# Optimization experiments

Measured on AMD Instinct MI355X. Metric: run time of the kernel, lower is better.

The kernel has to match this reference:

```python
import jax, jax.numpy as jnp
import numpy as np

N = 8192      # total factor-graph rows (detection nodes + association nodes)
ND = N // 2   # detection-node rows; rest are association (edge) rows
D_RAW = 74    # raw input dim; last 10 cols = convex hull (5 points x 2 coords)
EPS = 1e-5    # BatchNorm eps


def _adjs():
    # signed factor-graph adjacencies with self-loops marking row type
    rng = np.random.RandomState(0)
    deg = 8
    node_adj = np.zeros((N, N), np.float32)
    edge_adj = np.zeros((N, N), np.float32)
    nbr = rng.randint(ND, N, size=(ND, deg))
    node_adj[np.repeat(np.arange(ND), deg), nbr.ravel()] = rng.choice([-1.0, 1.0], ND * deg).astype(np.float32)
    node_adj[np.arange(ND), np.arange(ND)] = 1.0
    nbr2 = rng.randint(0, ND, size=(N - ND, deg))
    edge_adj[np.repeat(np.arange(ND, N), deg), nbr2.ravel()] = rng.choice([-1.0, 1.0], (N - ND) * deg).astype(np.float32)
    edge_adj[np.arange(ND, N), np.arange(ND, N)] = 1.0
    return jnp.asarray(node_adj), jnp.asarray(edge_adj)


def setup_inputs() -> dict:
    key = jax.random.key(0)
    ks = jax.random.split(key, 16)
    node_adj, edge_adj = _adjs()

    def lin(k, fi, fo):
        return jax.random.normal(k, (fi, fo), jnp.float32) / np.sqrt(fi)

    inp = {"x": jax.random.normal(ks[0], (N, D_RAW), jnp.float32),
           "node_adj": node_adj, "edge_adj": edge_adj}
    # PointNetfeatsmall: 1x1 conv stack 3->16->32->64 with eval-mode BatchNorm
    for i, (fi, fo) in enumerate([(3, 16), (16, 32), (32, 64)], 1):
        k = jax.random.split(ks[i], 5)
        inp[f"pn_w{i}"] = lin(k[0], fi, fo)
        inp[f"pn_b{i}"] = 0.1 * jax.random.normal(k[1], (fo,), jnp.float32)
        inp[f"pn_g{i}"] = 1.0 + 0.1 * jax.random.normal(k[2], (fo,), jnp.float32)
        inp[f"pn_be{i}"] = 0.1 * jax.random.normal(k[3], (fo,), jnp.float32)
        inp[f"pn_m{i}"] = 0.1 * jax.random.normal(k[4], (fo,), jnp.float32)
        inp[f"pn_v{i}"] = jnp.ones((fo,), jnp.float32)
    # FactorGraphConvolution weights (msg_type='concat' -> in dim doubles)
    for i, (fi, fo) in enumerate([(256, 64), (128, 64), (128, 1)], 1):
        k = jax.random.split(ks[10 + i], 2)
        inp[f"gc{i}_wn"] = lin(k[0], fi, fo)
        inp[f"gc{i}_we"] = lin(k[1], fi, fo)
        inp[f"gc{i}_bn"] = jnp.zeros((fo,), jnp.float32)
        inp[f"gc{i}_be"] = jnp.zeros((fo,), jnp.float32)
    inp["gc3_bn"] = jnp.full((1,), -4.595, jnp.float32)  # nn.init.constant_ in TrackMPNN.__init__
    inp["gc3_be"] = jnp.full((1,), 4.595, jnp.float32)
    return inp


def _bn(h, g, b, m, v):  # h: [N, C, P], eval-mode BatchNorm1d
    return (h - m[:, None]) * (g[:, None] / jnp.sqrt(v[:, None] + EPS)) + b[:, None]


def _fgc(h, node_adj, edge_adj, wn, we, bn_, be_, relu):
    # concat(self, aggregated-neighbors) -> linear; node/edge rows use their own branch
    node_out = jnp.concatenate([h, node_adj @ h], axis=1) @ wn + bn_
    edge_out = jnp.concatenate([h, edge_adj @ h], axis=1) @ we + be_
    out = jnp.where((jnp.diag(node_adj) != 0)[:, None], node_out, edge_out)
    return jax.nn.relu(out) if relu else out


def reference(x, node_adj, edge_adj,
              pn_w1, pn_b1, pn_g1, pn_be1, pn_m1, pn_v1,
              pn_w2, pn_b2, pn_g2, pn_be2, pn_m2, pn_v2,
              pn_w3, pn_b3, pn_g3, pn_be3, pn_m3, pn_v3,
              gc1_wn, gc1_we, gc1_bn, gc1_be,
              gc2_wn, gc2_we, gc2_bn, gc2_be,
              gc3_wn, gc3_we, gc3_bn, gc3_be):
    # convex hull branch: [N, 3, 5] (third coordinate zero-padded)
    ch = jnp.concatenate([x[:, -10:].reshape(-1, 2, 5),
                          jnp.zeros((x.shape[0], 1, 5), x.dtype)], axis=1)
    h = jax.nn.relu(_bn(jnp.einsum('ncp,cd->ndp', ch, pn_w1) + pn_b1[:, None], pn_g1, pn_be1, pn_m1, pn_v1))
    h = jax.nn.relu(_bn(jnp.einsum('ncp,cd->ndp', h, pn_w2) + pn_b2[:, None], pn_g2, pn_be2, pn_m2, pn_v2))
    h = _bn(jnp.einsum('ncp,cd->ndp', h, pn_w3) + pn_b3[:, None], pn_g3, pn_be3, pn_m3, pn_v3)
    feat = h.max(axis=2)                       # PointNet global max pool -> [N, 64]
    h = jnp.concatenate([x[:, :-10], feat], axis=1)  # [N, 128]
    h = _fgc(h, node_adj, edge_adj, gc1_wn, gc1_we, gc1_bn, gc1_be, True)
    h = _fgc(h, node_adj, edge_adj, gc2_wn, gc2_we, gc2_bn, gc2_be, True)
    h = _fgc(h, node_adj, edge_adj, gc3_wn, gc3_we, gc3_bn, gc3_be, False)
    return jax.nn.sigmoid(h)                   # [N, 1]
```

## Files before the change

### kernel.cpp

```cpp
#include <hip/hip_runtime.h>
#include <math.h>

#define NROWS 8192
#define NDET  4096

static constexpr int OFF_SGN = 65536;
static constexpr int OFF_PN  = 131072;
static constexpr int OFF_AGG = 655360;
static constexpr int OFF_H1  = 1703936;
static constexpr int OFF_H2  = 2228224;

__global__ __launch_bounds__(256) void k_extract(
    const float* __restrict__ nodeA, const float* __restrict__ edgeA,
    int* __restrict__ idx, float* __restrict__ sgn)
{
    int row = blockIdx.x, t = threadIdx.x;
    const float* src; int col0;
    if (row < NDET) { src = nodeA + (size_t)row * NROWS + NDET; col0 = NDET; }
    else            { src = edgeA + (size_t)row * NROWS;        col0 = 0;    }
    __shared__ int scnt;
    if (t == 0) scnt = 0;
    __syncthreads();
    const float4* s4 = (const float4*)src;
    #pragma unroll
    for (int it = 0; it < 4; ++it) {
        float4 v = s4[t + it * 256];
        int cb = col0 + (t + it * 256) * 4;
        if (v.x != 0.f) { int p = atomicAdd(&scnt, 1); idx[row * 8 + p] = cb;     sgn[row * 8 + p] = v.x; }
        if (v.y != 0.f) { int p = atomicAdd(&scnt, 1); idx[row * 8 + p] = cb + 1; sgn[row * 8 + p] = v.y; }
        if (v.z != 0.f) { int p = atomicAdd(&scnt, 1); idx[row * 8 + p] = cb + 2; sgn[row * 8 + p] = v.z; }
        if (v.w != 0.f) { int p = atomicAdd(&scnt, 1); idx[row * 8 + p] = cb + 3; sgn[row * 8 + p] = v.w; }
    }
    __syncthreads();
    for (int p = scnt + t; p < 8; p += 256) { idx[row * 8 + p] = 0; sgn[row * 8 + p] = 0.f; }
}

__global__ __launch_bounds__(256) void k_pointnet(
    const float* __restrict__ x,
    const float* __restrict__ w1, const float* __restrict__ b1,
    const float* __restrict__ g1, const float* __restrict__ be1,
    const float* __restrict__ m1, const float* __restrict__ v1,
    const float* __restrict__ w2, const float* __restrict__ b2,
    const float* __restrict__ g2, const float* __restrict__ be2,
    const float* __restrict__ m2, const float* __restrict__ v2,
    const float* __restrict__ w3, const float* __restrict__ b3,
    const float* __restrict__ g3, const float* __restrict__ be3,
    const float* __restrict__ m3, const float* __restrict__ v3,
    float* __restrict__ pn)
{
    __shared__ float fw[2720];
    int t = threadIdx.x;
    for (int i = t; i < 48; i += 256)  { int d = i & 15; fw[i]       = w1[i] * g1[d] * rsqrtf(v1[d] + 1e-5f); }
    for (int i = t; i < 16; i += 256)  {                 fw[48 + i]  = (b1[i] - m1[i]) * g1[i] * rsqrtf(v1[i] + 1e-5f) + be1[i]; }
    for (int i = t; i < 512; i += 256) { int d = i & 31; fw[64 + i]  = w2[i] * g2[d] * rsqrtf(v2[d] + 1e-5f); }
    for (int i = t; i < 32; i += 256)  {                 fw[576 + i] = (b2[i] - m2[i]) * g2[i] * rsqrtf(v2[i] + 1e-5f) + be2[i]; }
    for (int i = t; i < 2048; i += 256){ int d = i & 63; fw[608 + i] = w3[i] * g3[d] * rsqrtf(v3[d] + 1e-5f); }
    for (int i = t; i < 64; i += 256)  {                 fw[2656 + i]= (b3[i] - m3[i]) * g3[i] * rsqrtf(v3[i] + 1e-5f) + be3[i]; }
    __syncthreads();

    int lane = t & 63;
    int wv   = t >> 6;
    int l15  = lane & 15, l31 = lane & 31;
    int rowbase = (blockIdx.x * 4 + wv) * 4;

    for (int r = rowbase; r < rowbase + 4; ++r) {
        float val  = (lane < 10) ? x[(size_t)r * 74 + 64 + lane] : 0.f;
        float vmax = -3.0e38f;
        #pragma unroll
        for (int p = 0; p < 5; ++p) {
            float a0 = __shfl(val, p, 64);
            float a1 = __shfl(val, p + 5, 64);
            float h1v = fmaxf(0.f, a0 * fw[l15] + a1 * fw[16 + l15] + fw[48 + l15]);
            float s2 = fw[576 + l31];
            #pragma unroll
            for (int d = 0; d < 16; ++d)
                s2 += __shfl(h1v, d, 64) * fw[64 + d * 32 + l31];
            float h2v = fmaxf(0.f, s2);
            float s3 = fw[2656 + lane];
            #pragma unroll
            for (int e = 0; e < 32; ++e)
                s3 += __shfl(h2v, e, 64) * fw[608 + e * 64 + lane];
            vmax = fmaxf(vmax, s3);
        }
        pn[(size_t)r * 64 + lane] = vmax;
    }
}

__global__ __launch_bounds__(256) void k_gather1(
    const float* __restrict__ x, const float* __restrict__ pn,
    const int* __restrict__ idx, const float* __restrict__ sgn,
    float* __restrict__ agg)
{
    int lane = threadIdx.x & 63;
    int row  = blockIdx.x * 4 + (threadIdx.x >> 6);
    float acc0 = x[(size_t)row * 74 + lane];
    float acc1 = pn[(size_t)row * 64 + lane];
    #pragma unroll
    for (int j = 0; j < 8; ++j) {
        int nb   = idx[row * 8 + j];
        float sg = sgn[row * 8 + j];
        acc0 += sg * x[(size_t)nb * 74 + lane];
        acc1 += sg * pn[(size_t)nb * 64 + lane];
    }
    agg[(size_t)row * 128 + lane]      = acc0;
    agg[(size_t)row * 128 + 64 + lane] = acc1;
}

__global__ __launch_bounds__(256) void k_gather2(
    const float* __restrict__ h, const int* __restrict__ idx,
    const float* __restrict__ sgn, float* __restrict__ agg)
{
    int lane = threadIdx.x & 63;
    int row  = blockIdx.x * 4 + (threadIdx.x >> 6);
    float acc = h[(size_t)row * 64 + lane];
    #pragma unroll
    for (int j = 0; j < 8; ++j) {
        int nb   = idx[row * 8 + j];
        float sg = sgn[row * 8 + j];
        acc += sg * h[(size_t)nb * 64 + lane];
    }
    agg[(size_t)row * 64 + lane] = acc;
}

__global__ __launch_bounds__(256) void k_gemm1(
    const float* __restrict__ x, const float* __restrict__ pn,
    const float* __restrict__ agg,
    const float* __restrict__ wn, const float* __restrict__ we,
    const float* __restrict__ bn, const float* __restrict__ be,
    float* __restrict__ out)
{
    int r_l = threadIdx.x >> 2, cg = threadIdx.x & 3;
    int row = blockIdx.x * 64 + r_l;
    int c0  = blockIdx.y * 16 + cg * 4;
    bool isnode = blockIdx.x < 64;
    const float* W = isnode ? wn : we;
    const float* B = isnode ? bn : be;
    float acc[4] = {B[c0], B[c0 + 1], B[c0 + 2], B[c0 + 3]};

    const float2* x2 = (const float2*)(x + (size_t)row * 74);
    #pragma unroll
    for (int kg = 0; kg < 32; ++kg) {
        float2 v = x2[kg];
        float4 wv0 = *(const float4*)&W[(kg * 2) * 64 + c0];
        float4 wv1 = *(const float4*)&W[(kg * 2 + 1) * 64 + c0];
        acc[0] += v.x * wv0.x + v.y * wv1.x;
        acc[1] += v.x * wv0.y + v.y * wv1.y;
        acc[2] += v.x * wv0.z + v.y * wv1.z;
        acc[3] += v.x * wv0.w + v.y * wv1.w;
    }
    const float4* p4 = (const float4*)(pn + (size_t)row * 64);
    #pragma unroll
    for (int kg = 0; kg < 16; ++kg) {
        float4 v = p4[kg];
        const float* vv = &v.x;
        #pragma unroll
        for (int kk = 0; kk < 4; ++kk) {
            float4 wv = *(const float4*)&W[(64 + kg * 4 + kk) * 64 + c0];
            acc[0] += vv[kk] * wv.x; acc[1] += vv[kk] * wv.y;
            acc[2] += vv[kk] * wv.z; acc[3] += vv[kk] * wv.w;
        }
    }
    const float4* a4 = (const float4*)(agg + (size_t)row * 128);
    #pragma unroll
    for (int kg = 0; kg < 32; ++kg) {
        float4 v = a4[kg];
        const float* vv = &v.x;
        #pragma unroll
        for (int kk = 0; kk < 4; ++kk) {
            float4 wv = *(const float4*)&W[(128 + kg * 4 + kk) * 64 + c0];
            acc[0] += vv[kk] * wv.x; acc[1] += vv[kk] * wv.y;
            acc[2] += vv[kk] * wv.z; acc[3] += vv[kk] * wv.w;
        }
    }
    float4 o;
    o.x = fmaxf(acc[0], 0.f); o.y = fmaxf(acc[1], 0.f);
    o.z = fmaxf(acc[2], 0.f); o.w = fmaxf(acc[3], 0.f);
    *(float4*)&out[(size_t)row * 64 + c0] = o;
}

__global__ __launch_bounds__(256) void k_gemm2(
    const float* __restrict__ h, const float* __restrict__ agg,
    const float* __restrict__ wn, const float* __restrict__ we,
    const float* __restrict__ bn, const float* __restrict__ be,
    float* __restrict__ out)
{
    int r_l = threadIdx.x >> 2, cg = threadIdx.x & 3;
    int row = blockIdx.x * 64 + r_l;
    int c0  = blockIdx.y * 16 + cg * 4;
    bool isnode = blockIdx.x < 64;
    const float* W = isnode ? wn : we;
    const float* B = isnode ? bn : be;
    float acc[4] = {B[c0], B[c0 + 1], B[c0 + 2], B[c0 + 3]};

    const float4* h4 = (const float4*)(h + (size_t)row * 64);
    const float4* a4 = (const float4*)(agg + (size_t)row * 64);
    #pragma unroll
    for (int kg = 0; kg < 16; ++kg) {
        float4 v = h4[kg];
        const float* vv = &v.x;
        #pragma unroll
        for (int kk = 0; kk < 4; ++kk) {
            float4 wv = *(const float4*)&W[(kg * 4 + kk) * 64 + c0];
            acc[0] += vv[kk] * wv.x; acc[1] += vv[kk] * wv.y;
            acc[2] += vv[kk] * wv.z; acc[3] += vv[kk] * wv.w;
        }
    }
    #pragma unroll
    for (int kg = 0; kg < 16; ++kg) {
        float4 v = a4[kg];
        const float* vv = &v.x;
        #pragma unroll
        for (int kk = 0; kk < 4; ++kk) {
            float4 wv = *(const float4*)&W[(64 + kg * 4 + kk) * 64 + c0];
            acc[0] += vv[kk] * wv.x; acc[1] += vv[kk] * wv.y;
            acc[2] += vv[kk] * wv.z; acc[3] += vv[kk] * wv.w;
        }
    }
    float4 o;
    o.x = fmaxf(acc[0], 0.f); o.y = fmaxf(acc[1], 0.f);
    o.z = fmaxf(acc[2], 0.f); o.w = fmaxf(acc[3], 0.f);
    *(float4*)&out[(size_t)row * 64 + c0] = o;
}

__global__ __launch_bounds__(256) void k_gc3(
    const float* __restrict__ h2, const int* __restrict__ idx,
    const float* __restrict__ sgn,
    const float* __restrict__ wn, const float* __restrict__ we,
    const float* __restrict__ bn, const float* __restrict__ be,
    float* __restrict__ out)
{
    int lane = threadIdx.x & 63;
    int row  = blockIdx.x * 4 + (threadIdx.x >> 6);
    float own = h2[(size_t)row * 64 + lane];
    float agg = own;
    #pragma unroll
    for (int j = 0; j < 8; ++j) {
        int nb   = idx[row * 8 + j];
        float sg = sgn[row * 8 + j];
        agg += sg * h2[(size_t)nb * 64 + lane];
    }
    bool isnode = row < NDET;
    const float* w = isnode ? wn : we;
    float bias = isnode ? bn[0] : be[0];
    float acc = own * w[lane] + agg * w[64 + lane];
    #pragma unroll
    for (int off = 32; off > 0; off >>= 1)
        acc += __shfl_xor(acc, off, 64);
    if (lane == 0)
        out[row] = 1.f / (1.f + expf(-(acc + bias)));
}

extern "C" void kernel_launch(void* const* d_in, const int* in_sizes, int n_in,
                              void* d_out, int out_size, void* d_ws, size_t ws_size,
                              hipStream_t stream)
{
    const float* x     = (const float*)d_in[0];
    const float* nodeA = (const float*)d_in[1];
    const float* edgeA = (const float*)d_in[2];
    const float* pw1 = (const float*)d_in[3];  const float* pb1 = (const float*)d_in[4];
    const float* pg1 = (const float*)d_in[5];  const float* pe1 = (const float*)d_in[6];
    const float* pm1 = (const float*)d_in[7];  const float* pv1 = (const float*)d_in[8];
    const float* pw2 = (const float*)d_in[9];  const float* pb2 = (const float*)d_in[10];
    const float* pg2 = (const float*)d_in[11]; const float* pe2 = (const float*)d_in[12];
    const float* pm2 = (const float*)d_in[13]; const float* pv2 = (const float*)d_in[14];
    const float* pw3 = (const float*)d_in[15]; const float* pb3 = (const float*)d_in[16];
    const float* pg3 = (const float*)d_in[17]; const float* pe3 = (const float*)d_in[18];
    const float* pm3 = (const float*)d_in[19]; const float* pv3 = (const float*)d_in[20];
    const float* g1wn = (const float*)d_in[21]; const float* g1we = (const float*)d_in[22];
    const float* g1bn = (const float*)d_in[23]; const float* g1be = (const float*)d_in[24];
    const float* g2wn = (const float*)d_in[25]; const float* g2we = (const float*)d_in[26];
    const float* g2bn = (const float*)d_in[27]; const float* g2be = (const float*)d_in[28];
    const float* g3wn = (const float*)d_in[29]; const float* g3we = (const float*)d_in[30];
    const float* g3bn = (const float*)d_in[31]; const float* g3be = (const float*)d_in[32];

    float* ws  = (float*)d_ws;
    int*   idx = (int*)ws;
    float* sgn = ws + OFF_SGN;
    float* pn  = ws + OFF_PN;
    float* agg = ws + OFF_AGG;
    float* h1  = ws + OFF_H1;
    float* h2  = ws + OFF_H2;
    float* out = (float*)d_out;

    k_extract<<<NROWS, 256, 0, stream>>>(nodeA, edgeA, idx, sgn);
    k_pointnet<<<512, 256, 0, stream>>>(x,
        pw1, pb1, pg1, pe1, pm1, pv1,
        pw2, pb2, pg2, pe2, pm2, pv2,
        pw3, pb3, pg3, pe3, pm3, pv3, pn);
    k_gather1<<<2048, 256, 0, stream>>>(x, pn, idx, sgn, agg);
    k_gemm1<<<dim3(128, 4), 256, 0, stream>>>(x, pn, agg, g1wn, g1we, g1bn, g1be, h1);
    k_gather2<<<2048, 256, 0, stream>>>(h1, idx, sgn, agg);
    k_gemm2<<<dim3(128, 4), 256, 0, stream>>>(h1, agg, g2wn, g2we, g2bn, g2be, h2);
    k_gc3<<<2048, 256, 0, stream>>>(h2, idx, sgn, g3wn, g3we, g3bn, g3be, out);
}
```

Baseline: 554.2 us.

## Fuse gather into GEMM layers and merge extract with pointnet launch

Merges the adjacency extraction and PointNet kernels into one launch that picks its role from the block index. Fuses each neighbour-gather kernel into its following GEMM: 32-row aggregates are staged in shared memory instead of a global agg buffer, and each thread now computes 8 output columns. This drops two launches and a global round trip of the aggregates. In exchange the GEMM grid shrinks from 512 to 256 blocks, which lowers parallelism on a large GPU, and each block runs its gather serially before its GEMM.

```diff
diff --git a/kernel.cpp b/kernel.cpp
--- a/kernel.cpp
+++ b/kernel.cpp
@@ -6,36 +6,12 @@
 
 static constexpr int OFF_SGN = 65536;
 static constexpr int OFF_PN  = 131072;
-static constexpr int OFF_AGG = 655360;
 static constexpr int OFF_H1  = 1703936;
 static constexpr int OFF_H2  = 2228224;
 
-__global__ __launch_bounds__(256) void k_extract(
+__global__ __launch_bounds__(256) void k_front(
     const float* __restrict__ nodeA, const float* __restrict__ edgeA,
-    int* __restrict__ idx, float* __restrict__ sgn)
-{
-    int row = blockIdx.x, t = threadIdx.x;
-    const float* src; int col0;
-    if (row < NDET) { src = nodeA + (size_t)row * NROWS + NDET; col0 = NDET; }
-    else            { src = edgeA + (size_t)row * NROWS;        col0 = 0;    }
-    __shared__ int scnt;
-    if (t == 0) scnt = 0;
-    __syncthreads();
-    const float4* s4 = (const float4*)src;
-    #pragma unroll
-    for (int it = 0; it < 4; ++it) {
-        float4 v = s4[t + it * 256];
-        int cb = col0 + (t + it * 256) * 4;
-        if (v.x != 0.f) { int p = atomicAdd(&scnt, 1); idx[row * 8 + p] = cb;     sgn[row * 8 + p] = v.x; }
-        if (v.y != 0.f) { int p = atomicAdd(&scnt, 1); idx[row * 8 + p] = cb + 1; sgn[row * 8 + p] = v.y; }
-        if (v.z != 0.f) { int p = atomicAdd(&scnt, 1); idx[row * 8 + p] = cb + 2; sgn[row * 8 + p] = v.z; }
-        if (v.w != 0.f) { int p = atomicAdd(&scnt, 1); idx[row * 8 + p] = cb + 3; sgn[row * 8 + p] = v.w; }
-    }
-    __syncthreads();
-    for (int p = scnt + t; p < 8; p += 256) { idx[row * 8 + p] = 0; sgn[row * 8 + p] = 0.f; }
-}
-
-__global__ __launch_bounds__(256) void k_pointnet(
+    int* __restrict__ idx, float* __restrict__ sgn,
     const float* __restrict__ x,
     const float* __restrict__ w1, const float* __restrict__ b1,
     const float* __restrict__ g1, const float* __restrict__ be1,
@@ -48,8 +24,33 @@
     const float* __restrict__ m3, const float* __restrict__ v3,
     float* __restrict__ pn)
 {
+    __shared__ int scnt;
     __shared__ float fw[2720];
     int t = threadIdx.x;
+
+    if (blockIdx.x < NROWS) {
+        int row = blockIdx.x;
+        const float* src; int col0;
+        if (row < NDET) { src = nodeA + (size_t)row * NROWS + NDET; col0 = NDET; }
+        else            { src = edgeA + (size_t)row * NROWS;        col0 = 0;    }
+        if (t == 0) scnt = 0;
+        __syncthreads();
+        const float4* s4 = (const float4*)src;
+        #pragma unroll
+        for (int it = 0; it < 4; ++it) {
+            float4 v = s4[t + it * 256];
+            int cb = col0 + (t + it * 256) * 4;
+            if (v.x != 0.f) { int p = atomicAdd(&scnt, 1); idx[row * 8 + p] = cb;     sgn[row * 8 + p] = v.x; }
+            if (v.y != 0.f) { int p = atomicAdd(&scnt, 1); idx[row * 8 + p] = cb + 1; sgn[row * 8 + p] = v.y; }
+            if (v.z != 0.f) { int p = atomicAdd(&scnt, 1); idx[row * 8 + p] = cb + 2; sgn[row * 8 + p] = v.z; }
+            if (v.w != 0.f) { int p = atomicAdd(&scnt, 1); idx[row * 8 + p] = cb + 3; sgn[row * 8 + p] = v.w; }
+        }
+        __syncthreads();
+        for (int p = scnt + t; p < 8; p += 256) { idx[row * 8 + p] = 0; sgn[row * 8 + p] = 0.f; }
+        return;
+    }
+
+    int bp = blockIdx.x - NROWS;
     for (int i = t; i < 48; i += 256)  { int d = i & 15; fw[i]       = w1[i] * g1[d] * rsqrtf(v1[d] + 1e-5f); }
     for (int i = t; i < 16; i += 256)  {                 fw[48 + i]  = (b1[i] - m1[i]) * g1[i] * rsqrtf(v1[i] + 1e-5f) + be1[i]; }
     for (int i = t; i < 512; i += 256) { int d = i & 31; fw[64 + i]  = w2[i] * g2[d] * rsqrtf(v2[d] + 1e-5f); }
@@ -61,7 +62,7 @@
     int lane = t & 63;
     int wv   = t >> 6;
     int l15  = lane & 15, l31 = lane & 31;
-    int rowbase = (blockIdx.x * 4 + wv) * 4;
+    int rowbase = (bp * 4 + wv) * 4;
 
     for (int r = rowbase; r < rowbase + 4; ++r) {
         float val  = (lane < 10) ? x[(size_t)r * 74 + 64 + lane] : 0.f;
@@ -86,140 +87,142 @@
     }
 }
 
-__global__ __launch_bounds__(256) void k_gather1(
+__device__ __forceinline__ void fma8(float* acc, float s, const float* Wr)
+{
+    float4 wa = *(const float4*)Wr;
+    float4 wb = *(const float4*)(Wr + 4);
+    acc[0] += s * wa.x; acc[1] += s * wa.y; acc[2] += s * wa.z; acc[3] += s * wa.w;
+    acc[4] += s * wb.x; acc[5] += s * wb.y; acc[6] += s * wb.z; acc[7] += s * wb.w;
+}
+
+__global__ __launch_bounds__(256) void k_layer1(
     const float* __restrict__ x, const float* __restrict__ pn,
     const int* __restrict__ idx, const float* __restrict__ sgn,
-    float* __restrict__ agg)
-{
-    int lane = threadIdx.x & 63;
-    int row  = blockIdx.x * 4 + (threadIdx.x >> 6);
-    float acc0 = x[(size_t)row * 74 + lane];
-    float acc1 = pn[(size_t)row * 64 + lane];
-    #pragma unroll
-    for (int j = 0; j < 8; ++j) {
-        int nb   = idx[row * 8 + j];
-        float sg = sgn[row * 8 + j];
-        acc0 += sg * x[(size_t)nb * 74 + lane];
-        acc1 += sg * pn[(size_t)nb * 64 + lane];
-    }
-    agg[(size_t)row * 128 + lane]      = acc0;
-    agg[(size_t)row * 128 + 64 + lane] = acc1;
-}
-
-__global__ __launch_bounds__(256) void k_gather2(
-    const float* __restrict__ h, const int* __restrict__ idx,
-    const float* __restrict__ sgn, float* __restrict__ agg)
-{
-    int lane = threadIdx.x & 63;
-    int row  = blockIdx.x * 4 + (threadIdx.x >> 6);
-    float acc = h[(size_t)row * 64 + lane];
-    #pragma unroll
-    for (int j = 0; j < 8; ++j) {
-        int nb   = idx[row * 8 + j];
-        float sg = sgn[row * 8 + j];
-        acc += sg * h[(size_t)nb * 64 + lane];
-    }
-    agg[(size_t)row * 64 + lane] = acc;
-}
-
-__global__ __launch_bounds__(256) void k_gemm1(
-    const float* __restrict__ x, const float* __restrict__ pn,
-    const float* __restrict__ agg,
     const float* __restrict__ wn, const float* __restrict__ we,
     const float* __restrict__ bn, const float* __restrict__ be,
     float* __restrict__ out)
 {
-    int r_l = threadIdx.x >> 2, cg = threadIdx.x & 3;
-    int row = blockIdx.x * 64 + r_l;
-    int c0  = blockIdx.y * 16 + cg * 4;
-    bool isnode = blockIdx.x < 64;
+    __shared__ float aggL[32 * 132];
+    int t = threadIdx.x;
+    int base = blockIdx.x * 32;
+    int lane = t & 63, wv = t >> 6;
+
+    for (int i = 0; i < 8; ++i) {
+        int rl = wv * 8 + i;
+        int row = base + rl;
+        float acc0 = x[(size_t)row * 74 + lane];
+        float acc1 = pn[(size_t)row * 64 + lane];
+        #pragma unroll
+        for (int j = 0; j < 8; ++j) {
+            int nb   = idx[row * 8 + j];
+            float sg = sgn[row * 8 + j];
+            acc0 += sg * x[(size_t)nb * 74 + lane];
+            acc1 += sg * pn[(size_t)nb * 64 + lane];
+        }
+        aggL[rl * 132 + lane]      = acc0;
+        aggL[rl * 132 + 64 + lane] = acc1;
+    }
+    __syncthreads();
+
+    int r_l = t >> 3, cg = t & 7;
+    int row = base + r_l;
+    int c0  = cg * 8;
+    bool isnode = blockIdx.x < 128;
     const float* W = isnode ? wn : we;
     const float* B = isnode ? bn : be;
-    float acc[4] = {B[c0], B[c0 + 1], B[c0 + 2], B[c0 + 3]};
+    float acc[8];
+    #pragma unroll
+    for (int c = 0; c < 8; ++c) acc[c] = B[c0 + c];
 
     const float2* x2 = (const float2*)(x + (size_t)row * 74);
     #pragma unroll
     for (int kg = 0; kg < 32; ++kg) {
         float2 v = x2[kg];
-        float4 wv0 = *(const float4*)&W[(kg * 2) * 64 + c0];
-        float4 wv1 = *(const float4*)&W[(kg * 2 + 1) * 64 + c0];
-        acc[0] += v.x * wv0.x + v.y * wv1.x;
-        acc[1] += v.x * wv0.y + v.y * wv1.y;
-        acc[2] += v.x * wv0.z + v.y * wv1.z;
-        acc[3] += v.x * wv0.w + v.y * wv1.w;
+        fma8(acc, v.x, &W[(kg * 2) * 64 + c0]);
+        fma8(acc, v.y, &W[(kg * 2 + 1) * 64 + c0]);
     }
     const float4* p4 = (const float4*)(pn + (size_t)row * 64);
     #pragma unroll
     for (int kg = 0; kg < 16; ++kg) {
         float4 v = p4[kg];
-        const float* vv = &v.x;
-        #pragma unroll
-        for (int kk = 0; kk < 4; ++kk) {
-            float4 wv = *(const float4*)&W[(64 + kg * 4 + kk) * 64 + c0];
-            acc[0] += vv[kk] * wv.x; acc[1] += vv[kk] * wv.y;
-            acc[2] += vv[kk] * wv.z; acc[3] += vv[kk] * wv.w;
-        }
-    }
-    const float4* a4 = (const float4*)(agg + (size_t)row * 128);
+        fma8(acc, v.x, &W[(64 + kg * 4)     * 64 + c0]);
+        fma8(acc, v.y, &W[(64 + kg * 4 + 1) * 64 + c0]);
+        fma8(acc, v.z, &W[(64 + kg * 4 + 2) * 64 + c0]);
+        fma8(acc, v.w, &W[(64 + kg * 4 + 3) * 64 + c0]);
+    }
     #pragma unroll
     for (int kg = 0; kg < 32; ++kg) {
-        float4 v = a4[kg];
-        const float* vv = &v.x;
-        #pragma unroll
-        for (int kk = 0; kk < 4; ++kk) {
-            float4 wv = *(const float4*)&W[(128 + kg * 4 + kk) * 64 + c0];
-            acc[0] += vv[kk] * wv.x; acc[1] += vv[kk] * wv.y;
-            acc[2] += vv[kk] * wv.z; acc[3] += vv[kk] * wv.w;
-        }
-    }
-    float4 o;
-    o.x = fmaxf(acc[0], 0.f); o.y = fmaxf(acc[1], 0.f);
-    o.z = fmaxf(acc[2], 0.f); o.w = fmaxf(acc[3], 0.f);
-    *(float4*)&out[(size_t)row * 64 + c0] = o;
-}
-
-__global__ __launch_bounds__(256) void k_gemm2(
-    const float* __restrict__ h, const float* __restrict__ agg,
+        float4 v = *(const float4*)&aggL[r_l * 132 + kg * 4];
+        fma8(acc, v.x, &W[(128 + kg * 4)     * 64 + c0]);
+        fma8(acc, v.y, &W[(128 + kg * 4 + 1) * 64 + c0]);
+        fma8(acc, v.z, &W[(128 + kg * 4 + 2) * 64 + c0]);
+        fma8(acc, v.w, &W[(128 + kg * 4 + 3) * 64 + c0]);
+    }
+    float4 o0, o1;
+    o0.x = fmaxf(acc[0], 0.f); o0.y = fmaxf(acc[1], 0.f); o0.z = fmaxf(acc[2], 0.f); o0.w = fmaxf(acc[3], 0.f);
+    o1.x = fmaxf(acc[4], 0.f); o1.y = fmaxf(acc[5], 0.f); o1.z = fmaxf(acc[6], 0.f); o1.w = fmaxf(acc[7], 0.f);
+    *(float4*)&out[(size_t)row * 64 + c0]     = o0;
+    *(float4*)&out[(size_t)row * 64 + c0 + 4] = o1;
+}
+
+__global__ __launch_bounds__(256) void k_layer2(
+    const float* __restrict__ h, const int* __restrict__ idx,
+    const float* __restrict__ sgn,
     const float* __restrict__ wn, const float* __restrict__ we,
     const float* __restrict__ bn, const float* __restrict__ be,
     float* __restrict__ out)
 {
-    int r_l = threadIdx.x >> 2, cg = threadIdx.x & 3;
-    int row = blockIdx.x * 64 + r_l;
-    int c0  = blockIdx.y * 16 + cg * 4;
-    bool isnode = blockIdx.x < 64;
+    __shared__ float aggL[32 * 68];
+    int t = threadIdx.x;
+    int base = blockIdx.x * 32;
+    int lane = t & 63, wv = t >> 6;
+
+    for (int i = 0; i < 8; ++i) {
+        int rl = wv * 8 + i;
+        int row = base + rl;
+        float acc = h[(size_t)row * 64 + lane];
+        #pragma unroll
+        for (int j = 0; j < 8; ++j) {
+            int nb   = idx[row * 8 + j];
+            float sg = sgn[row * 8 + j];
+            acc += sg * h[(size_t)nb * 64 + lane];
+        }
+        aggL[rl * 68 + lane] = acc;
+    }
+    __syncthreads();
+
+    int r_l = t >> 3, cg = t & 7;
+    int row = base + r_l;
+    int c0  = cg * 8;
+    bool isnode = blockIdx.x < 128;
     const float* W = isnode ? wn : we;
     const float* B = isnode ? bn : be;
-    float acc[4] = {B[c0], B[c0 + 1], B[c0 + 2], B[c0 + 3]};
+    float acc[8];
+    #pragma unroll
+    for (int c = 0; c < 8; ++c) acc[c] = B[c0 + c];
 
     const float4* h4 = (const float4*)(h + (size_t)row * 64);
-    const float4* a4 = (const float4*)(agg + (size_t)row * 64);
     #pragma unroll
     for (int kg = 0; kg < 16; ++kg) {
         float4 v = h4[kg];
-        const float* vv = &v.x;
-        #pragma unroll
-        for (int kk = 0; kk < 4; ++kk) {
-            float4 wv = *(const float4*)&W[(kg * 4 + kk) * 64 + c0];
-            acc[0] += vv[kk] * wv.x; acc[1] += vv[kk] * wv.y;
-            acc[2] += vv[kk] * wv.z; acc[3] += vv[kk] * wv.w;
-        }
+        fma8(acc, v.x, &W[(kg * 4)     * 64 + c0]);
+        fma8(acc, v.y, &W[(kg * 4 + 1) * 64 + c0]);
+        fma8(acc, v.z, &W[(kg * 4 + 2) * 64 + c0]);
+        fma8(acc, v.w, &W[(kg * 4 + 3) * 64 + c0]);
     }
     #pragma unroll
     for (int kg = 0; kg < 16; ++kg) {
-        float4 v = a4[kg];
-        const float* vv = &v.x;
-        #pragma unroll
-        for (int kk = 0; kk < 4; ++kk) {
-            float4 wv = *(const float4*)&W[(64 + kg * 4 + kk) * 64 + c0];
-            acc[0] += vv[kk] * wv.x; acc[1] += vv[kk] * wv.y;
-            acc[2] += vv[kk] * wv.z; acc[3] += vv[kk] * wv.w;
-        }
-    }
-    float4 o;
-    o.x = fmaxf(acc[0], 0.f); o.y = fmaxf(acc[1], 0.f);
-    o.z = fmaxf(acc[2], 0.f); o.w = fmaxf(acc[3], 0.f);
-    *(float4*)&out[(size_t)row * 64 + c0] = o;
+        float4 v = *(const float4*)&aggL[r_l * 68 + kg * 4];
+        fma8(acc, v.x, &W[(64 + kg * 4)     * 64 + c0]);
+        fma8(acc, v.y, &W[(64 + kg * 4 + 1) * 64 + c0]);
+        fma8(acc, v.z, &W[(64 + kg * 4 + 2) * 64 + c0]);
+        fma8(acc, v.w, &W[(64 + kg * 4 + 3) * 64 + c0]);
+    }
+    float4 o0, o1;
+    o0.x = fmaxf(acc[0], 0.f); o0.y = fmaxf(acc[1], 0.f); o0.z = fmaxf(acc[2], 0.f); o0.w = fmaxf(acc[3], 0.f);
+    o1.x = fmaxf(acc[4], 0.f); o1.y = fmaxf(acc[5], 0.f); o1.z = fmaxf(acc[6], 0.f); o1.w = fmaxf(acc[7], 0.f);
+    *(float4*)&out[(size_t)row * 64 + c0]     = o0;
+    *(float4*)&out[(size_t)row * 64 + c0 + 4] = o1;
 }
 
 __global__ __launch_bounds__(256) void k_gc3(
@@ -277,19 +280,15 @@
     int*   idx = (int*)ws;
     float* sgn = ws + OFF_SGN;
     float* pn  = ws + OFF_PN;
-    float* agg = ws + OFF_AGG;
     float* h1  = ws + OFF_H1;
     float* h2  = ws + OFF_H2;
     float* out = (float*)d_out;
 
-    k_extract<<<NROWS, 256, 0, stream>>>(nodeA, edgeA, idx, sgn);
-    k_pointnet<<<512, 256, 0, stream>>>(x,
+    k_front<<<NROWS + 512, 256, 0, stream>>>(nodeA, edgeA, idx, sgn, x,
         pw1, pb1, pg1, pe1, pm1, pv1,
         pw2, pb2, pg2, pe2, pm2, pv2,
         pw3, pb3, pg3, pe3, pm3, pv3, pn);
-    k_gather1<<<2048, 256, 0, stream>>>(x, pn, idx, sgn, agg);
-    k_gemm1<<<dim3(128, 4), 256, 0, stream>>>(x, pn, agg, g1wn, g1we, g1bn, g1be, h1);
-    k_gather2<<<2048, 256, 0, stream>>>(h1, idx, sgn, agg);
-    k_gemm2<<<dim3(128, 4), 256, 0, stream>>>(h1, agg, g2wn, g2we, g2bn, g2be, h2);
+    k_layer1<<<256, 256, 0, stream>>>(x, pn, idx, sgn, g1wn, g1we, g1bn, g1be, h1);
+    k_layer2<<<256, 256, 0, stream>>>(h1, idx, sgn, g2wn, g2we, g2bn, g2be, h2);
     k_gc3<<<2048, 256, 0, stream>>>(h2, idx, sgn, g3wn, g3we, g3bn, g3be, out);
 }
```

Measured after the change: 578.9 us. +4.4%, slower.
